# Optimization experiments

Hardware: AMD Instinct MI355X
Metric: run time of the kernel (lower is better)

The kernel has to match this reference:

```python
import jax, jax.numpy as jnp
import numpy as np

N = 100000   # nodes (single node type 'word')
R = 4        # relation types (sorted rel_names)
E = 160000   # edges per relation
H = 128      # h_dim
O = 64       # out_dim


def setup_inputs() -> dict:
    key = jax.random.key(0)
    k0, k1, k2, k3 = jax.random.split(key, 4)
    embed = jax.random.normal(k0, (N, H), jnp.float32) * 0.1          # RelGraphEmbed table
    weight = jax.random.normal(k1, (R, H, O), jnp.float32) / np.sqrt(H)  # layer-2 per-rel weight
    bias1 = jnp.zeros((H,), jnp.float32)   # layer-1 h_bias
    bias2 = jnp.zeros((O,), jnp.float32)   # layer-2 h_bias
    edge_src = jax.random.randint(k2, (R, E), 0, N)
    edge_dst = jax.random.randint(k3, (R, E), 0, N)
    return dict(embed=embed, weight=weight, bias1=bias1, bias2=bias2,
                edge_src=edge_src, edge_dst=edge_dst)


def _rel_mean(x, src, dst, num_nodes):
    # GraphConv(norm='right'): sum messages into dst, divide by dst in-degree.
    msg = x[src]                                                    # [E, d] gather
    summed = jax.ops.segment_sum(msg, dst, num_segments=num_nodes)  # scatter-add
    deg = jax.ops.segment_sum(jnp.ones(src.shape, x.dtype), dst, num_segments=num_nodes)
    return summed / jnp.maximum(deg, 1.0)[:, None]


def reference(embed, weight, bias1, bias2, edge_src, edge_dst):
    n = embed.shape[0]
    # Layer 1: weight=False -> HeteroGraphConv sums right-normalized aggregations, then bias+relu.
    h1 = jnp.zeros_like(embed)
    for r in range(edge_src.shape[0]):
        h1 = h1 + _rel_mean(embed, edge_src[r], edge_dst[r], n)
    h1 = jax.nn.relu(h1 + bias1)
    # Layer 2: per-relation linear transform, aggregate, sum over relations, bias (no activation).
    out = jnp.zeros((n, weight.shape[-1]), embed.dtype)
    for r in range(edge_src.shape[0]):
        out = out + _rel_mean(h1 @ weight[r], edge_src[r], edge_dst[r], n)
    return out + bias2
```

## Files before the change

### kernel.cpp

```cpp
#include <hip/hip_runtime.h>
#include <hip/hip_bf16.h>

#define H 128
#define O 64
#define RELS 4

typedef short short8 __attribute__((ext_vector_type(8)));
typedef float f32x4 __attribute__((ext_vector_type(4)));

static __device__ __forceinline__ unsigned short f2b(float x) {
    __hip_bfloat16 h = __float2bfloat16(x);
    return *reinterpret_cast<unsigned short*>(&h);
}
static __device__ __forceinline__ float blo(unsigned u) { return __uint_as_float(u << 16); }
static __device__ __forceinline__ float bhi(unsigned u) { return __uint_as_float(u & 0xffff0000u); }

#define ACC8(acc, uv, wt)                                           \
    acc[0] += (wt) * blo(uv.x); acc[1] += (wt) * bhi(uv.x);         \
    acc[2] += (wt) * blo(uv.y); acc[3] += (wt) * bhi(uv.y);         \
    acc[4] += (wt) * blo(uv.z); acc[5] += (wt) * bhi(uv.z);         \
    acc[6] += (wt) * blo(uv.w); acc[7] += (wt) * bhi(uv.w);

__global__ void k_prep(const float* __restrict__ embed, unsigned short* __restrict__ eb,
                       const float* __restrict__ W, unsigned short* __restrict__ WT,
                       const int* __restrict__ dst, int* __restrict__ cnt,
                       int n4, int wtot, int E, int RE, int N, int b_cvt, int b_w) {
    int b = blockIdx.x;
    if (b < b_cvt) {
        int i = b * 256 + threadIdx.x;
        if (i < n4) {
            float4 v = ((const float4*)embed)[i];
            ushort4 o;
            o.x = f2b(v.x); o.y = f2b(v.y); o.z = f2b(v.z); o.w = f2b(v.w);
            ((ushort4*)eb)[i] = o;
        }
    } else if (b < b_cvt + b_w) {
        int i = (b - b_cvt) * 256 + threadIdx.x;
        if (i < wtot) {
            int r = i >> 13;
            int n = (i >> 7) & (O - 1);
            int k = i & (H - 1);
            WT[i] = f2b(W[((size_t)r * H + k) * O + n]);
        }
    } else {
        int i = (b - b_cvt - b_w) * 256 + threadIdx.x;
        if (i < RE) { int r = i / E; atomicAdd(&cnt[r * N + dst[i]], 1); }
    }
}

__global__ void k_scan1(const int* __restrict__ cnt, int* __restrict__ offs,
                        int* __restrict__ bsum, int n, int N_) {
    __shared__ int sh[256];
    int t = threadIdx.x;
    int base = blockIdx.x * 1024 + t * 4;
    int4 v = make_int4(0, 0, 0, 0);
    if (base + 3 < n && (N_ & 3) == 0) {
#pragma unroll
        for (int r = 0; r < RELS; ++r) {
            int4 c = *(const int4*)(cnt + (size_t)r * N_ + base);
            v.x += c.x; v.y += c.y; v.z += c.z; v.w += c.w;
        }
    } else {
        for (int j = 0; j < 4; ++j) {
            int i = base + j;
            if (i < n) {
                int s = 0;
                for (int r = 0; r < RELS; ++r) s += cnt[(size_t)r * N_ + i];
                (&v.x)[j] = s;
            }
        }
    }
    int s = v.x + v.y + v.z + v.w;
    sh[t] = s; __syncthreads();
    for (int off = 1; off < 256; off <<= 1) {
        int x = (t >= off) ? sh[t - off] : 0;
        __syncthreads();
        sh[t] += x;
        __syncthreads();
    }
    int incl = sh[t];
    int ex = incl - s;
    if (base < n)     offs[base]     = ex;
    if (base + 1 < n) offs[base + 1] = ex + v.x;
    if (base + 2 < n) offs[base + 2] = ex + v.x + v.y;
    if (base + 3 < n) offs[base + 3] = ex + v.x + v.y + v.z;
    if (t == 255) bsum[blockIdx.x] = incl;
}

__global__ void k_scan2(int* __restrict__ bsum, int nb) {
    __shared__ int sh[512];
    int t = threadIdx.x;
    int s = (t < nb) ? bsum[t] : 0;
    sh[t] = s; __syncthreads();
    for (int off = 1; off < 512; off <<= 1) {
        int x = (t >= off) ? sh[t - off] : 0;
        __syncthreads();
        sh[t] += x;
        __syncthreads();
    }
    if (t < nb) bsum[t] = sh[t] - s;
}

__global__ void k_scan3c(int* __restrict__ offs, const int* __restrict__ bsum,
                         const int* __restrict__ cnt, int* __restrict__ cursor,
                         int n, int total, int N_) {
    int i = blockIdx.x * blockDim.x + threadIdx.x;
    if (i < n) {
        int off = offs[i] + bsum[i >> 10];
        offs[i] = off;
        int c0 = cnt[i], c1 = cnt[N_ + i], c2 = cnt[2 * N_ + i];
        cursor[i]          = off;
        cursor[N_ + i]     = off + c0;
        cursor[2 * N_ + i] = off + c0 + c1;
        cursor[3 * N_ + i] = off + c0 + c1 + c2;
    }
    if (i == 0) offs[n] = total;
}

__global__ void k_fill(const int* __restrict__ src, const int* __restrict__ dst,
                       const int* __restrict__ cnt, int* __restrict__ cursor,
                       uint2* __restrict__ ue, int E, int RE, int N) {
    int i = blockIdx.x * blockDim.x + threadIdx.x;
    if (i >= RE) return;
    int r = i / E;
    int d = dst[i];
    int pos = atomicAdd(&cursor[r * N + d], 1);
    float w = 1.0f / (float)max(cnt[r * N + d], 1);
    ue[pos] = make_uint2((unsigned)(r * N + src[i]), __float_as_uint(w));
}

__global__ void k_pull1(const unsigned short* __restrict__ eb, const int* __restrict__ offs2,
                        const uint2* __restrict__ ue, const float* __restrict__ bias1,
                        unsigned short* __restrict__ h1, int N) {
    int node = blockIdx.x * 16 + (threadIdx.x >> 4);
    if (node >= N) return;
    int q = threadIdx.x & 15;
    int beg = offs2[node], end = offs2[node + 1];
    unsigned N1 = (unsigned)N, N2 = (unsigned)(2 * N);

    float a[8] = {0.f, 0.f, 0.f, 0.f, 0.f, 0.f, 0.f, 0.f};
    float c[8] = {0.f, 0.f, 0.f, 0.f, 0.f, 0.f, 0.f, 0.f};

    int e = beg;
    for (; e + 2 <= end; e += 2) {
        uint2 p0 = ue[e], p1 = ue[e + 1];
        unsigned s0 = p0.x; if (s0 >= N2) s0 -= N2; if (s0 >= N1) s0 -= N1;
        unsigned s1 = p1.x; if (s1 >= N2) s1 -= N2; if (s1 >= N1) s1 -= N1;
        float w0 = __uint_as_float(p0.y), w1 = __uint_as_float(p1.y);
        uint4 u0 = *(const uint4*)(eb + (size_t)s0 * H + q * 8);
        uint4 u1 = *(const uint4*)(eb + (size_t)s1 * H + q * 8);
        ACC8(a, u0, w0);
        ACC8(c, u1, w1);
    }
    if (e < end) {
        uint2 p0 = ue[e];
        unsigned s0 = p0.x; if (s0 >= N2) s0 -= N2; if (s0 >= N1) s0 -= N1;
        float w0 = __uint_as_float(p0.y);
        uint4 u0 = *(const uint4*)(eb + (size_t)s0 * H + q * 8);
        ACC8(a, u0, w0);
    }

    float4 b0 = *(const float4*)(bias1 + q * 8);
    float4 b1 = *(const float4*)(bias1 + q * 8 + 4);
    float f0 = fmaxf(a[0] + c[0] + b0.x, 0.f);
    float f1 = fmaxf(a[1] + c[1] + b0.y, 0.f);
    float f2 = fmaxf(a[2] + c[2] + b0.z, 0.f);
    float f3 = fmaxf(a[3] + c[3] + b0.w, 0.f);
    float f4 = fmaxf(a[4] + c[4] + b1.x, 0.f);
    float f5 = fmaxf(a[5] + c[5] + b1.y, 0.f);
    float f6 = fmaxf(a[6] + c[6] + b1.z, 0.f);
    float f7 = fmaxf(a[7] + c[7] + b1.w, 0.f);
    uint4 o;
    o.x = (unsigned)f2b(f0) | ((unsigned)f2b(f1) << 16);
    o.y = (unsigned)f2b(f2) | ((unsigned)f2b(f3) << 16);
    o.z = (unsigned)f2b(f4) | ((unsigned)f2b(f5) << 16);
    o.w = (unsigned)f2b(f6) | ((unsigned)f2b(f7) << 16);
    *(uint4*)(h1 + (size_t)node * H + q * 8) = o;
}

__global__ __launch_bounds__(256) void k_gemm(const unsigned short* __restrict__ h1,
                                              const unsigned short* __restrict__ WT,
                                              unsigned short* __restrict__ T, int N) {
    __shared__ __align__(16) unsigned short st[4][32][72];
    int tid = threadIdx.x, w = tid >> 6, l = tid & 63;
    int row0 = blockIdx.x * 128 + w * 32;
    int rA = l & 15, kb = (l >> 4) * 8;

    short8 af[2][4];
#pragma unroll
    for (int mf = 0; mf < 2; ++mf)
#pragma unroll
        for (int kk = 0; kk < 4; ++kk) {
            int row = row0 + mf * 16 + rA;
            short8 v = {0, 0, 0, 0, 0, 0, 0, 0};
            if (row < N) v = *(const short8*)(h1 + (size_t)row * H + kk * 32 + kb);
            af[mf][kk] = v;
        }

    for (int r = 0; r < RELS; ++r) {
        f32x4 z = {0.f, 0.f, 0.f, 0.f};
        f32x4 acc[2][4];
#pragma unroll
        for (int mf = 0; mf < 2; ++mf)
#pragma unroll
            for (int nt = 0; nt < 4; ++nt) acc[mf][nt] = z;

#pragma unroll
        for (int nt = 0; nt < 4; ++nt) {
            short8 bf[4];
#pragma unroll
            for (int kk = 0; kk < 4; ++kk)
                bf[kk] = *(const short8*)(WT + (((size_t)r * O + nt * 16 + rA) * H + kk * 32 + kb));
#pragma unroll
            for (int kk = 0; kk < 4; ++kk)
#pragma unroll
                for (int mf = 0; mf < 2; ++mf)
                    acc[mf][nt] = __builtin_amdgcn_mfma_f32_16x16x32_bf16(
                        af[mf][kk], bf[kk], acc[mf][nt], 0, 0, 0);
        }

#pragma unroll
        for (int mf = 0; mf < 2; ++mf)
#pragma unroll
            for (int nt = 0; nt < 4; ++nt)
#pragma unroll
                for (int j = 0; j < 4; ++j)
                    st[w][mf * 16 + (l >> 4) * 4 + j][nt * 16 + (l & 15)] = f2b(acc[mf][nt][j]);

#pragma unroll
        for (int i = 0; i < 4; ++i) {
            int rr = i * 8 + (l >> 3);
            uint4 v = *(const uint4*)&st[w][rr][(l & 7) * 8];
            int grow = row0 + rr;
            if (grow < N)
                *(uint4*)(T + ((size_t)r * N + grow) * O + (l & 7) * 8) = v;
        }
    }
}

__global__ void k_pull2(const unsigned short* __restrict__ T, const int* __restrict__ offs2,
                        const uint2* __restrict__ ue, const float* __restrict__ bias2,
                        float* __restrict__ out, int N) {
    int node = blockIdx.x * 32 + (threadIdx.x >> 3);
    if (node >= N) return;
    int o = threadIdx.x & 7;
    int beg = offs2[node], end = offs2[node + 1];

    float a[8] = {0.f, 0.f, 0.f, 0.f, 0.f, 0.f, 0.f, 0.f};
    float c[8] = {0.f, 0.f, 0.f, 0.f, 0.f, 0.f, 0.f, 0.f};

    int e = beg;
    for (; e + 2 <= end; e += 2) {
        uint2 p0 = ue[e], p1 = ue[e + 1];
        float w0 = __uint_as_float(p0.y), w1 = __uint_as_float(p1.y);
        uint4 u0 = *(const uint4*)(T + (size_t)p0.x * O + o * 8);
        uint4 u1 = *(const uint4*)(T + (size_t)p1.x * O + o * 8);
        ACC8(a, u0, w0);
        ACC8(c, u1, w1);
    }
    if (e < end) {
        uint2 p0 = ue[e];
        float w0 = __uint_as_float(p0.y);
        uint4 u0 = *(const uint4*)(T + (size_t)p0.x * O + o * 8);
        ACC8(a, u0, w0);
    }

    float4 b0 = *(const float4*)(bias2 + o * 8);
    float4 b1 = *(const float4*)(bias2 + o * 8 + 4);
    float4 v0, v1;
    v0.x = a[0] + c[0] + b0.x; v0.y = a[1] + c[1] + b0.y;
    v0.z = a[2] + c[2] + b0.z; v0.w = a[3] + c[3] + b0.w;
    v1.x = a[4] + c[4] + b1.x; v1.y = a[5] + c[5] + b1.y;
    v1.z = a[6] + c[6] + b1.z; v1.w = a[7] + c[7] + b1.w;
    *(float4*)(out + (size_t)node * O + o * 8)     = v0;
    *(float4*)(out + (size_t)node * O + o * 8 + 4) = v1;
}

extern "C" void kernel_launch(void* const* d_in, const int* in_sizes, int n_in,
                              void* d_out, int out_size, void* d_ws, size_t ws_size,
                              hipStream_t stream) {
    const float* embed  = (const float*)d_in[0];
    const float* weight = (const float*)d_in[1];
    const float* bias1  = (const float*)d_in[2];
    const float* bias2  = (const float*)d_in[3];
    const int*   esrc   = (const int*)d_in[4];
    const int*   edst   = (const int*)d_in[5];
    float* out = (float*)d_out;

    const int N = in_sizes[0] / H;
    const int E = in_sizes[4] / RELS;
    const int RN = RELS * N;
    const int RE = RELS * E;

    char* p = (char*)d_ws;
    auto alloc = [&](size_t bytes) {
        char* q = p;
        p += (bytes + 255) & ~(size_t)255;
        return q;
    };
    int* cnt    = (int*)alloc((size_t)RN * 4);
    int* offs2  = (int*)alloc(((size_t)N + 1) * 4);
    int* cursor = (int*)alloc((size_t)RN * 4);
    int* bsum   = (int*)alloc(4096);
    uint2* ue   = (uint2*)alloc((size_t)RE * 8);
    unsigned short* eb  = (unsigned short*)alloc((size_t)N * H * 2);
    unsigned short* h1  = (unsigned short*)alloc((size_t)N * H * 2);
    unsigned short* WT  = (unsigned short*)alloc((size_t)RELS * O * H * 2);
    unsigned short* T   = (unsigned short*)alloc((size_t)RELS * N * O * 2);

    hipMemsetAsync(cnt, 0, (size_t)RN * 4, stream);

    int n4 = N * H / 4;
    int wtot = RELS * O * H;
    int b_cvt = (n4 + 255) / 256;
    int b_w   = (wtot + 255) / 256;
    int b_h   = (RE + 255) / 256;
    k_prep<<<b_cvt + b_w + b_h, 256, 0, stream>>>(embed, eb, weight, WT, edst, cnt,
                                                  n4, wtot, E, RE, N, b_cvt, b_w);

    int nb = (N + 1023) / 1024;
    k_scan1<<<nb, 256, 0, stream>>>(cnt, offs2, bsum, N, N);
    k_scan2<<<1, 512, 0, stream>>>(bsum, nb);
    k_scan3c<<<(N + 255) / 256, 256, 0, stream>>>(offs2, bsum, cnt, cursor, N, RE, N);

    k_fill<<<(RE + 255) / 256, 256, 0, stream>>>(esrc, edst, cnt, cursor, ue, E, RE, N);

    k_pull1<<<(N + 15) / 16, 256, 0, stream>>>(eb, offs2, ue, bias1, h1, N);

    k_gemm<<<(N + 127) / 128, 256, 0, stream>>>(h1, WT, T, N);

    k_pull2<<<(N + 31) / 32, 256, 0, stream>>>(T, offs2, ue, bias2, out, N);
}
```

Measured before the change: 176.4 us.

## Fuse layer-2 aggregate-then-transform into one kernel using per-relation MFMA

Layer 2 is reordered to aggregate h1 rows per relation first and then multiply by that relation's weight. Each wave gathers 128-wide bf16 rows for 16 nodes, converts the sums to bf16 fragments and accumulates all four relations in MFMA registers before writing fp32 output. This drops the separate GEMM kernel, the intermediate T buffer (R*N*O bf16) and the second pull pass. In exchange it gathers 128-wide rows instead of 64-wide, needs 32 fp32 accumulators per lane, and relies on cursor/cnt holding per-relation segment ends and on ue sources being offset by r*N. The embedding conversion blocks are also changed so each thread handles four float4 elements.

```diff
diff --git a/kernel.cpp b/kernel.cpp
--- a/kernel.cpp
+++ b/kernel.cpp
@@ -21,26 +21,37 @@
     acc[4] += (wt) * blo(uv.z); acc[5] += (wt) * bhi(uv.z);         \
     acc[6] += (wt) * blo(uv.w); acc[7] += (wt) * bhi(uv.w);
 
+#define ACC8B(acc, B_, uv, wt)                                              \
+    acc[(B_)+0] += (wt) * blo(uv.x); acc[(B_)+1] += (wt) * bhi(uv.x);       \
+    acc[(B_)+2] += (wt) * blo(uv.y); acc[(B_)+3] += (wt) * bhi(uv.y);       \
+    acc[(B_)+4] += (wt) * blo(uv.z); acc[(B_)+5] += (wt) * bhi(uv.z);       \
+    acc[(B_)+6] += (wt) * blo(uv.w); acc[(B_)+7] += (wt) * bhi(uv.w);
+
 __global__ void k_prep(const float* __restrict__ embed, unsigned short* __restrict__ eb,
-                       const float* __restrict__ W, unsigned short* __restrict__ WT,
+                       const float* __restrict__ W, unsigned short* __restrict__ WT2,
                        const int* __restrict__ dst, int* __restrict__ cnt,
                        int n4, int wtot, int E, int RE, int N, int b_cvt, int b_w) {
     int b = blockIdx.x;
     if (b < b_cvt) {
-        int i = b * 256 + threadIdx.x;
-        if (i < n4) {
-            float4 v = ((const float4*)embed)[i];
-            ushort4 o;
-            o.x = f2b(v.x); o.y = f2b(v.y); o.z = f2b(v.z); o.w = f2b(v.w);
-            ((ushort4*)eb)[i] = o;
+        int base = b * 1024;
+#pragma unroll
+        for (int k = 0; k < 4; ++k) {
+            int i = base + k * 256 + threadIdx.x;
+            if (i < n4) {
+                float4 v = ((const float4*)embed)[i];
+                ushort4 o;
+                o.x = f2b(v.x); o.y = f2b(v.y); o.z = f2b(v.z); o.w = f2b(v.w);
+                ((ushort4*)eb)[i] = o;
+            }
         }
     } else if (b < b_cvt + b_w) {
         int i = (b - b_cvt) * 256 + threadIdx.x;
         if (i < wtot) {
-            int r = i >> 13;
-            int n = (i >> 7) & (O - 1);
-            int k = i & (H - 1);
-            WT[i] = f2b(W[((size_t)r * H + k) * O + n]);
+            int n = i >> 9;
+            int kcat = i & 511;
+            int r = kcat >> 7;
+            int k = kcat & (H - 1);
+            WT2[i] = f2b(W[((size_t)r * H + k) * O + n]);
         }
     } else {
         int i = (b - b_cvt - b_w) * 256 + threadIdx.x;
@@ -178,102 +189,93 @@
     *(uint4*)(h1 + (size_t)node * H + q * 8) = o;
 }
 
-__global__ __launch_bounds__(256) void k_gemm(const unsigned short* __restrict__ h1,
-                                              const unsigned short* __restrict__ WT,
-                                              unsigned short* __restrict__ T, int N) {
-    __shared__ __align__(16) unsigned short st[4][32][72];
-    int tid = threadIdx.x, w = tid >> 6, l = tid & 63;
-    int row0 = blockIdx.x * 128 + w * 32;
-    int rA = l & 15, kb = (l >> 4) * 8;
-
-    short8 af[2][4];
-#pragma unroll
-    for (int mf = 0; mf < 2; ++mf)
-#pragma unroll
-        for (int kk = 0; kk < 4; ++kk) {
-            int row = row0 + mf * 16 + rA;
-            short8 v = {0, 0, 0, 0, 0, 0, 0, 0};
-            if (row < N) v = *(const short8*)(h1 + (size_t)row * H + kk * 32 + kb);
-            af[mf][kk] = v;
-        }
+__global__ __launch_bounds__(256) void k_l2(const unsigned short* __restrict__ h1,
+                                            const int* __restrict__ cursor,
+                                            const int* __restrict__ cnt,
+                                            const uint2* __restrict__ ue,
+                                            const unsigned short* __restrict__ WT2,
+                                            const float* __restrict__ bias2,
+                                            float* __restrict__ out, int N) {
+    int l = threadIdx.x & 63;
+    int wv = threadIdx.x >> 6;
+    int node0 = blockIdx.x * 64 + wv * 16;
+    int rA = l & 15, q = l >> 4;
+    int node = node0 + rA;
+
+    f32x4 z = {0.f, 0.f, 0.f, 0.f};
+    f32x4 cacc[4] = {z, z, z, z};
 
     for (int r = 0; r < RELS; ++r) {
-        f32x4 z = {0.f, 0.f, 0.f, 0.f};
-        f32x4 acc[2][4];
-#pragma unroll
-        for (int mf = 0; mf < 2; ++mf)
-#pragma unroll
-            for (int nt = 0; nt < 4; ++nt) acc[mf][nt] = z;
-
-#pragma unroll
-        for (int nt = 0; nt < 4; ++nt) {
-            short8 bf[4];
-#pragma unroll
-            for (int kk = 0; kk < 4; ++kk)
-                bf[kk] = *(const short8*)(WT + (((size_t)r * O + nt * 16 + rA) * H + kk * 32 + kb));
-#pragma unroll
-            for (int kk = 0; kk < 4; ++kk)
-#pragma unroll
-                for (int mf = 0; mf < 2; ++mf)
-                    acc[mf][nt] = __builtin_amdgcn_mfma_f32_16x16x32_bf16(
-                        af[mf][kk], bf[kk], acc[mf][nt], 0, 0, 0);
-        }
-
-#pragma unroll
-        for (int mf = 0; mf < 2; ++mf)
-#pragma unroll
-            for (int nt = 0; nt < 4; ++nt)
-#pragma unroll
-                for (int j = 0; j < 4; ++j)
-                    st[w][mf * 16 + (l >> 4) * 4 + j][nt * 16 + (l & 15)] = f2b(acc[mf][nt][j]);
-
-#pragma unroll
-        for (int i = 0; i < 4; ++i) {
-            int rr = i * 8 + (l >> 3);
-            uint4 v = *(const uint4*)&st[w][rr][(l & 7) * 8];
-            int grow = row0 + rr;
-            if (grow < N)
-                *(uint4*)(T + ((size_t)r * N + grow) * O + (l & 7) * 8) = v;
-        }
-    }
-}
-
-__global__ void k_pull2(const unsigned short* __restrict__ T, const int* __restrict__ offs2,
-                        const uint2* __restrict__ ue, const float* __restrict__ bias2,
-                        float* __restrict__ out, int N) {
-    int node = blockIdx.x * 32 + (threadIdx.x >> 3);
-    if (node >= N) return;
-    int o = threadIdx.x & 7;
-    int beg = offs2[node], end = offs2[node + 1];
-
-    float a[8] = {0.f, 0.f, 0.f, 0.f, 0.f, 0.f, 0.f, 0.f};
-    float c[8] = {0.f, 0.f, 0.f, 0.f, 0.f, 0.f, 0.f, 0.f};
-
-    int e = beg;
-    for (; e + 2 <= end; e += 2) {
-        uint2 p0 = ue[e], p1 = ue[e + 1];
-        float w0 = __uint_as_float(p0.y), w1 = __uint_as_float(p1.y);
-        uint4 u0 = *(const uint4*)(T + (size_t)p0.x * O + o * 8);
-        uint4 u1 = *(const uint4*)(T + (size_t)p1.x * O + o * 8);
-        ACC8(a, u0, w0);
-        ACC8(c, u1, w1);
-    }
-    if (e < end) {
-        uint2 p0 = ue[e];
-        float w0 = __uint_as_float(p0.y);
-        uint4 u0 = *(const uint4*)(T + (size_t)p0.x * O + o * 8);
-        ACC8(a, u0, w0);
-    }
-
-    float4 b0 = *(const float4*)(bias2 + o * 8);
-    float4 b1 = *(const float4*)(bias2 + o * 8 + 4);
-    float4 v0, v1;
-    v0.x = a[0] + c[0] + b0.x; v0.y = a[1] + c[1] + b0.y;
-    v0.z = a[2] + c[2] + b0.z; v0.w = a[3] + c[3] + b0.w;
-    v1.x = a[4] + c[4] + b1.x; v1.y = a[5] + c[5] + b1.y;
-    v1.z = a[6] + c[6] + b1.z; v1.w = a[7] + c[7] + b1.w;
-    *(float4*)(out + (size_t)node * O + o * 8)     = v0;
-    *(float4*)(out + (size_t)node * O + o * 8 + 4) = v1;
+        int rN = r * N;
+        int end_ = 0, c_ = 0;
+        if (node < N) { end_ = cursor[rN + node]; c_ = cnt[rN + node]; }
+        int beg = end_ - c_;
+
+        float acc[32];
+#pragma unroll
+        for (int i = 0; i < 32; ++i) acc[i] = 0.f;
+
+        int e = beg;
+        for (; e + 2 <= end_; e += 2) {
+            uint2 p0 = ue[e], p1 = ue[e + 1];
+            unsigned s0 = p0.x - (unsigned)rN;
+            unsigned s1 = p1.x - (unsigned)rN;
+            float w0 = __uint_as_float(p0.y), w1 = __uint_as_float(p1.y);
+            const unsigned short* r0 = h1 + (size_t)s0 * H + q * 8;
+            const unsigned short* r1 = h1 + (size_t)s1 * H + q * 8;
+            uint4 u0 = *(const uint4*)(r0);
+            uint4 u1 = *(const uint4*)(r0 + 32);
+            uint4 u2 = *(const uint4*)(r0 + 64);
+            uint4 u3 = *(const uint4*)(r0 + 96);
+            uint4 v0 = *(const uint4*)(r1);
+            uint4 v1 = *(const uint4*)(r1 + 32);
+            uint4 v2 = *(const uint4*)(r1 + 64);
+            uint4 v3 = *(const uint4*)(r1 + 96);
+            ACC8B(acc, 0,  u0, w0); ACC8B(acc, 8,  u1, w0);
+            ACC8B(acc, 16, u2, w0); ACC8B(acc, 24, u3, w0);
+            ACC8B(acc, 0,  v0, w1); ACC8B(acc, 8,  v1, w1);
+            ACC8B(acc, 16, v2, w1); ACC8B(acc, 24, v3, w1);
+        }
+        if (e < end_) {
+            uint2 p0 = ue[e];
+            unsigned s0 = p0.x - (unsigned)rN;
+            float w0 = __uint_as_float(p0.y);
+            const unsigned short* r0 = h1 + (size_t)s0 * H + q * 8;
+            uint4 u0 = *(const uint4*)(r0);
+            uint4 u1 = *(const uint4*)(r0 + 32);
+            uint4 u2 = *(const uint4*)(r0 + 64);
+            uint4 u3 = *(const uint4*)(r0 + 96);
+            ACC8B(acc, 0,  u0, w0); ACC8B(acc, 8,  u1, w0);
+            ACC8B(acc, 16, u2, w0); ACC8B(acc, 24, u3, w0);
+        }
+
+        short8 af[4];
+#pragma unroll
+        for (int kk = 0; kk < 4; ++kk)
+#pragma unroll
+            for (int j = 0; j < 8; ++j)
+                af[kk][j] = (short)f2b(acc[kk * 8 + j]);
+
+#pragma unroll
+        for (int kk = 0; kk < 4; ++kk)
+#pragma unroll
+            for (int nt = 0; nt < 4; ++nt) {
+                short8 bf = *(const short8*)(WT2 + ((size_t)(nt * 16 + rA)) * 512
+                                             + r * H + kk * 32 + q * 8);
+                cacc[nt] = __builtin_amdgcn_mfma_f32_16x16x32_bf16(af[kk], bf, cacc[nt], 0, 0, 0);
+            }
+    }
+
+#pragma unroll
+    for (int nt = 0; nt < 4; ++nt) {
+        int col = nt * 16 + rA;
+        float b2 = bias2[col];
+#pragma unroll
+        for (int j = 0; j < 4; ++j) {
+            int nrow = node0 + q * 4 + j;
+            if (nrow < N) out[(size_t)nrow * O + col] = cacc[nt][j] + b2;
+        }
+    }
 }
 
 extern "C" void kernel_launch(void* const* d_in, const int* in_sizes, int n_in,
@@ -305,17 +307,16 @@
     uint2* ue   = (uint2*)alloc((size_t)RE * 8);
     unsigned short* eb  = (unsigned short*)alloc((size_t)N * H * 2);
     unsigned short* h1  = (unsigned short*)alloc((size_t)N * H * 2);
-    unsigned short* WT  = (unsigned short*)alloc((size_t)RELS * O * H * 2);
-    unsigned short* T   = (unsigned short*)alloc((size_t)RELS * N * O * 2);
+    unsigned short* WT2 = (unsigned short*)alloc((size_t)O * RELS * H * 2);
 
     hipMemsetAsync(cnt, 0, (size_t)RN * 4, stream);
 
     int n4 = N * H / 4;
-    int wtot = RELS * O * H;
-    int b_cvt = (n4 + 255) / 256;
+    int wtot = O * RELS * H;
+    int b_cvt = (n4 + 1023) / 1024;
     int b_w   = (wtot + 255) / 256;
     int b_h   = (RE + 255) / 256;
-    k_prep<<<b_cvt + b_w + b_h, 256, 0, stream>>>(embed, eb, weight, WT, edst, cnt,
+    k_prep<<<b_cvt + b_w + b_h, 256, 0, stream>>>(embed, eb, weight, WT2, edst, cnt,
                                                   n4, wtot, E, RE, N, b_cvt, b_w);
 
     int nb = (N + 1023) / 1024;
@@ -327,7 +328,5 @@
 
     k_pull1<<<(N + 15) / 16, 256, 0, stream>>>(eb, offs2, ue, bias1, h1, N);
 
-    k_gemm<<<(N + 127) / 128, 256, 0, stream>>>(h1, WT, T, N);
-
-    k_pull2<<<(N + 31) / 32, 256, 0, stream>>>(T, offs2, ue, bias2, out, N);
-}
+    k_l2<<<(N + 63) / 64, 256, 0, stream>>>(h1, cursor, cnt, ue, WT2, bias2, out, N);
+}
```

Measured after the change: 208.7 us. 1.18x slower.
